# Performance work log

Measured on AMD Instinct MI355X. Metric: run time of the kernel, lower is better.

## Reference

```python
import math
import jax, jax.numpy as jnp
import numpy as np

N, D = 16384, 1024


def setup_inputs() -> dict:
    key = jax.random.key(0)
    k1, k2 = jax.random.split(key)
    return {
        "image_embeddings_aligned": jax.random.normal(k1, (N, D), dtype=jnp.float32),
        "text_embeddings_aligned": jax.random.normal(k2, (N, D), dtype=jnp.float32),
        "logit_scale": jnp.asarray(math.log(20.0), dtype=jnp.float32),  # stored as log(init)
        "logit_bias": jnp.asarray(-10.0, dtype=jnp.float32),
    }


def _l2_normalize(x, eps=1e-12):
    # matches F.normalize(p=2, dim=-1)
    n = jnp.linalg.norm(x, axis=-1, keepdims=True)
    return x / jnp.maximum(n, eps)


def reference(image_embeddings_aligned, text_embeddings_aligned, logit_scale, logit_bias):
    img = _l2_normalize(image_embeddings_aligned)
    txt = _l2_normalize(text_embeddings_aligned)
    # [N, N] pairwise logits
    logits = jnp.exp(logit_scale) * jnp.einsum("nd,md->nm", img, txt) + logit_bias
    n = logits.shape[0]
    labels = 2.0 * jnp.eye(n, dtype=logits.dtype) - 1.0  # +1 on diagonal, -1 off
    loss_matrix = jax.nn.log_sigmoid(labels * logits)
    siglip_loss = -jnp.mean(loss_matrix)  # total_loss (structure_lambda == 0)
    return siglip_loss
```

## Files before the change

### kernel.cpp

```cpp
#include <hip/hip_runtime.h>

#define NROWS 16384
#define DIM   1024
#define QSCALE 32.0f
#define E8M0S  0x7A7A7A7Au

typedef int    v4i    __attribute__((ext_vector_type(4)));
typedef int    v8i    __attribute__((ext_vector_type(8)));
typedef float  f32x16 __attribute__((ext_vector_type(16)));

__device__ __forceinline__ void glds16(const void* g, void* l) {
    __builtin_amdgcn_global_load_lds(
        (const __attribute__((address_space(1))) void*)g,
        (__attribute__((address_space(3))) void*)l,
        16, 0, 0);
}

__device__ __forceinline__ float fexp2(float x) {
#if __has_builtin(__builtin_amdgcn_exp2f)
    return __builtin_amdgcn_exp2f(x);
#else
    return exp2f(x);
#endif
}
__device__ __forceinline__ float flog2(float x) {
#if __has_builtin(__builtin_amdgcn_logf)
    return __builtin_amdgcn_logf(x);
#else
    return log2f(x);
#endif
}

__device__ __forceinline__ unsigned fp4_nib(float y) {
    unsigned s = (__float_as_uint(y) >> 31) << 3;
    float a = fminf(fabsf(y), 6.0f);
    unsigned c = (unsigned)(a >= 0.25f) + (unsigned)(a >= 0.75f) +
                 (unsigned)(a >= 1.25f) + (unsigned)(a >= 1.75f) +
                 (unsigned)(a >= 2.5f)  + (unsigned)(a >= 3.5f)  +
                 (unsigned)(a >= 5.0f);
    return c | s;
}

__global__ __launch_bounds__(256) void norm_fused(
    const float* __restrict__ img,
    const float* __restrict__ txt,
    unsigned char* __restrict__ imgQ,
    unsigned char* __restrict__ txtQ,
    const float* __restrict__ lscale,
    const float* __restrict__ lbias,
    float* __restrict__ diagPart) {
    const int t    = threadIdx.x;
    const int lane = t & 63;
    const int r31  = lane & 31;
    const int half = lane >> 5;
    const int gw   = blockIdx.x * 4 + (t >> 6);
    const int row  = gw * 2 + half;
    const float sc   = __expf(lscale[0]);
    const float bias = lbias[0];

    const float4* pi = (const float4*)(img + (size_t)row * DIM) + r31 * 8;
    const float4* pt = (const float4*)(txt + (size_t)row * DIM) + r31 * 8;
    float4 vi[8], vt[8];
    float ssi = 0.0f, sst = 0.0f, dot = 0.0f;
    #pragma unroll
    for (int j = 0; j < 8; ++j) {
        vi[j] = pi[j];
        vt[j] = pt[j];
        ssi += vi[j].x*vi[j].x + vi[j].y*vi[j].y + vi[j].z*vi[j].z + vi[j].w*vi[j].w;
        sst += vt[j].x*vt[j].x + vt[j].y*vt[j].y + vt[j].z*vt[j].z + vt[j].w*vt[j].w;
        dot += vi[j].x*vt[j].x + vi[j].y*vt[j].y + vi[j].z*vt[j].z + vi[j].w*vt[j].w;
    }
    #pragma unroll
    for (int off = 1; off < 32; off <<= 1) {
        ssi += __shfl_xor(ssi, off, 64);
        sst += __shfl_xor(sst, off, 64);
        dot += __shfl_xor(dot, off, 64);
    }
    const float ii = 1.0f / fmaxf(sqrtf(ssi), 1e-12f);
    const float it = 1.0f / fmaxf(sqrtf(sst), 1e-12f);
    if (r31 == 0) diagPart[row] = -fmaf(sc, dot * ii * it, bias);

    const float qi = ii * QSCALE, qt = it * QSCALE;
    unsigned wp[4] = {0, 0, 0, 0}, wq[4] = {0, 0, 0, 0};
    #pragma unroll
    for (int j = 0; j < 8; ++j) {
        unsigned p = fp4_nib(vi[j].x * qi)       | (fp4_nib(vi[j].y * qi) << 4) |
                     (fp4_nib(vi[j].z * qi) << 8) | (fp4_nib(vi[j].w * qi) << 12);
        unsigned q = fp4_nib(vt[j].x * qt)       | (fp4_nib(vt[j].y * qt) << 4) |
                     (fp4_nib(vt[j].z * qt) << 8) | (fp4_nib(vt[j].w * qt) << 12);
        wp[j >> 1] |= p << ((j & 1) * 16);
        wq[j >> 1] |= q << ((j & 1) * 16);
    }
    const size_t qoff = ((size_t)(row >> 5) * 32 + r31) * 512 + (row & 31) * 16;
    *(v4i*)(imgQ + qoff) = *(v4i*)wp;
    *(v4i*)(txtQ + qoff) = *(v4i*)wq;
}

__global__ __launch_bounds__(256, 4) void siglip_gemm(
    const unsigned char* __restrict__ A,
    const unsigned char* __restrict__ B,
    const float* __restrict__ lscale,
    const float* __restrict__ lbias,
    float* __restrict__ gemmPart)
{
    __shared__ unsigned char sA[2][16 * 1024];
    __shared__ float wred[4];

    const int t    = threadIdx.x;
    const int lane = t & 63;
    const int wave = t >> 6;
    const int wr   = wave >> 1;
    const int wc   = wave & 1;

    const int b    = blockIdx.x;
    const int xcd  = b & 7;
    const int lb   = b >> 3;
    const int bcol = xcd * 16 + (lb & 15);
    const int brow = lb >> 4;

    const unsigned char* Aw = A + ((size_t)(brow * 4 + wave) * 32) * 512
                                + (size_t)lane * 16;
    const unsigned char* Bw = B + ((size_t)(bcol * 4 + wc * 2) * 32) * 512
                                + (size_t)lane * 16;

    f32x16 acc[2][2] = {};

    #pragma unroll
    for (int s = 0; s < 4; ++s)
        glds16(Aw + (size_t)(s * 2) * 512, sA[0] + (wave * 8 + s * 2) * 512);
    __syncthreads();

    #pragma unroll
    for (int k = 0; k < 4; ++k) {
        const int cur = k & 1;

        if (k < 3) {
            #pragma unroll
            for (int s = 0; s < 4; ++s)
                glds16(Aw + (size_t)((k + 1) * 8 + s * 2) * 512,
                       sA[cur ^ 1] + (wave * 8 + s * 2) * 512);
        }

        v4i bc0 = *(const v4i*)(Bw + (size_t)(k * 8) * 512);
        v4i bc1 = *(const v4i*)(Bw + 16384 + (size_t)(k * 8) * 512);

        #pragma unroll
        for (int ks = 0; ks < 4; ++ks) {
            v4i bn0, bn1;
            if (ks < 3) {
                bn0 = *(const v4i*)(Bw + (size_t)(k * 8 + (ks + 1) * 2) * 512);
                bn1 = *(const v4i*)(Bw + 16384 + (size_t)(k * 8 + (ks + 1) * 2) * 512);
            }
            v4i a0 = *(const v4i*)(sA[cur] + ((2 * wr + 0) * 8 + ks * 2) * 512 + lane * 16);
            v4i a1 = *(const v4i*)(sA[cur] + ((2 * wr + 1) * 8 + ks * 2) * 512 + lane * 16);

            v8i A0 = __builtin_shufflevector(a0, a0, 0, 1, 2, 3, -1, -1, -1, -1);
            v8i A1 = __builtin_shufflevector(a1, a1, 0, 1, 2, 3, -1, -1, -1, -1);
            v8i B0 = __builtin_shufflevector(bc0, bc0, 0, 1, 2, 3, -1, -1, -1, -1);
            v8i B1 = __builtin_shufflevector(bc1, bc1, 0, 1, 2, 3, -1, -1, -1, -1);

            __builtin_amdgcn_s_setprio(1);
            acc[0][0] = __builtin_amdgcn_mfma_scale_f32_32x32x64_f8f6f4(
                A0, B0, acc[0][0], 4, 4, 0, (int)E8M0S, 0, (int)E8M0S);
            acc[0][1] = __builtin_amdgcn_mfma_scale_f32_32x32x64_f8f6f4(
                A0, B1, acc[0][1], 4, 4, 0, (int)E8M0S, 0, (int)E8M0S);
            acc[1][0] = __builtin_amdgcn_mfma_scale_f32_32x32x64_f8f6f4(
                A1, B0, acc[1][0], 4, 4, 0, (int)E8M0S, 0, (int)E8M0S);
            acc[1][1] = __builtin_amdgcn_mfma_scale_f32_32x32x64_f8f6f4(
                A1, B1, acc[1][1], 4, 4, 0, (int)E8M0S, 0, (int)E8M0S);
            __builtin_amdgcn_s_setprio(0);

            if (ks < 3) { bc0 = bn0; bc1 = bn1; }
        }

        __syncthreads();
    }

    const float l2e   = 1.44269504088896341f;
    const float scale = __expf(lscale[0]);
    const float aCo   = scale * l2e;
    const float bCo   = lbias[0] * l2e;
    float local = 0.0f;
    #pragma unroll
    for (int mi = 0; mi < 2; ++mi)
        #pragma unroll
        for (int ni = 0; ni < 2; ++ni)
            #pragma unroll
            for (int r = 0; r < 16; r += 4) {
                float e0 = fexp2(fmaf(aCo, acc[mi][ni][r + 0], bCo));
                float e1 = fexp2(fmaf(aCo, acc[mi][ni][r + 1], bCo));
                float e2 = fexp2(fmaf(aCo, acc[mi][ni][r + 2], bCo));
                float e3 = fexp2(fmaf(aCo, acc[mi][ni][r + 3], bCo));
                float p  = ((1.0f + e0) * (1.0f + e1)) *
                           ((1.0f + e2) * (1.0f + e3));
                local += flog2(p);
            }

    #pragma unroll
    for (int off = 32; off > 0; off >>= 1) local += __shfl_down(local, off, 64);
    if (lane == 0) wred[wave] = local;
    __syncthreads();
    if (t == 0)
        gemmPart[blockIdx.x] =
            (wred[0] + wred[1] + wred[2] + wred[3]) * 0.69314718055994531f;
}

__global__ __launch_bounds__(1024) void finalize_kernel(
    const float* __restrict__ parts, float* __restrict__ out) {
    __shared__ float wr[16];
    const int t    = threadIdx.x;
    const int lane = t & 63;
    const int wave = t >> 6;
    const float4* p4 = (const float4*)parts;
    float s = 0.0f;
    for (int i = t; i < 8192; i += 1024) {
        float4 v = p4[i];
        s += v.x + v.y + v.z + v.w;
    }
    #pragma unroll
    for (int off = 32; off > 0; off >>= 1) s += __shfl_down(s, off, 64);
    if (lane == 0) wr[wave] = s;
    __syncthreads();
    if (t == 0) {
        float tot = 0.0f;
        #pragma unroll
        for (int i = 0; i < 16; ++i) tot += wr[i];
        out[0] = tot / 268435456.0f;
    }
}

extern "C" void kernel_launch(void* const* d_in, const int* in_sizes, int n_in,
                              void* d_out, int out_size, void* d_ws, size_t ws_size,
                              hipStream_t stream) {
    const float* img    = (const float*)d_in[0];
    const float* txt    = (const float*)d_in[1];
    const float* lscale = (const float*)d_in[2];
    const float* lbias  = (const float*)d_in[3];
    float* out = (float*)d_out;

    char* ws = (char*)d_ws;
    unsigned char* imgQ = (unsigned char*)ws;
    unsigned char* txtQ = (unsigned char*)(ws + (size_t)NROWS * 512);
    float* parts   = (float*)(ws + (size_t)2 * NROWS * 512);
    float* diagPart = parts;
    float* gemmPart = parts + NROWS;

    norm_fused<<<2048, 256, 0, stream>>>(img, txt, imgQ, txtQ, lscale, lbias, diagPart);
    siglip_gemm<<<dim3((NROWS / 128) * (NROWS / 128)), 256, 0, stream>>>(
        imgQ, txtQ, lscale, lbias, gemmPart);
    finalize_kernel<<<1, 1024, 0, stream>>>(parts, out);
}
```

Before: 313.1 us.

## Load A fragments directly from global into registers, dropping LDS staging

Removes the LDS double buffer and global_load_lds staging for the A operand. Each wave now loads both A and B fragments straight from global memory into registers, with a one-step register prefetch across a 16-step K loop, so the __syncthreads barriers go away. This cuts LDS traffic and synchronisation, but each A tile is now fetched by two waves instead of being shared through LDS, which doubles global/L2 reads for A.

Result: no change. 310.1 us (-1.0%).

```diff
diff --git a/kernel.cpp b/kernel.cpp
--- a/kernel.cpp
+++ b/kernel.cpp
@@ -8,13 +8,6 @@
 typedef int    v4i    __attribute__((ext_vector_type(4)));
 typedef int    v8i    __attribute__((ext_vector_type(8)));
 typedef float  f32x16 __attribute__((ext_vector_type(16)));
-
-__device__ __forceinline__ void glds16(const void* g, void* l) {
-    __builtin_amdgcn_global_load_lds(
-        (const __attribute__((address_space(1))) void*)g,
-        (__attribute__((address_space(3))) void*)l,
-        16, 0, 0);
-}
 
 __device__ __forceinline__ float fexp2(float x) {
 #if __has_builtin(__builtin_amdgcn_exp2f)
@@ -103,14 +96,13 @@
     const float* __restrict__ lbias,
     float* __restrict__ gemmPart)
 {
-    __shared__ unsigned char sA[2][16 * 1024];
     __shared__ float wred[4];
 
     const int t    = threadIdx.x;
     const int lane = t & 63;
     const int wave = t >> 6;
-    const int wr   = wave >> 1;
-    const int wc   = wave & 1;
+    const int wy   = wave >> 1;
+    const int wx   = wave & 1;
 
     const int b    = blockIdx.x;
     const int xcd  = b & 7;
@@ -118,62 +110,46 @@
     const int bcol = xcd * 16 + (lb & 15);
     const int brow = lb >> 4;
 
-    const unsigned char* Aw = A + ((size_t)(brow * 4 + wave) * 32) * 512
+    const unsigned char* Ab = A + (size_t)(brow * 4 + wy * 2) * 16384
                                 + (size_t)lane * 16;
-    const unsigned char* Bw = B + ((size_t)(bcol * 4 + wc * 2) * 32) * 512
+    const unsigned char* Bb = B + (size_t)(bcol * 4 + wx * 2) * 16384
                                 + (size_t)lane * 16;
 
     f32x16 acc[2][2] = {};
 
-    #pragma unroll
-    for (int s = 0; s < 4; ++s)
-        glds16(Aw + (size_t)(s * 2) * 512, sA[0] + (wave * 8 + s * 2) * 512);
-    __syncthreads();
-
-    #pragma unroll
-    for (int k = 0; k < 4; ++k) {
-        const int cur = k & 1;
-
-        if (k < 3) {
-            #pragma unroll
-            for (int s = 0; s < 4; ++s)
-                glds16(Aw + (size_t)((k + 1) * 8 + s * 2) * 512,
-                       sA[cur ^ 1] + (wave * 8 + s * 2) * 512);
+    v4i a0 = *(const v4i*)(Ab);
+    v4i a1 = *(const v4i*)(Ab + 16384);
+    v4i b0 = *(const v4i*)(Bb);
+    v4i b1 = *(const v4i*)(Bb + 16384);
+
+    #pragma unroll
+    for (int s = 0; s < 16; ++s) {
+        v4i na0, na1, nb0, nb1;
+        if (s < 15) {
+            const int o = (s + 1) * 1024;
+            na0 = *(const v4i*)(Ab + o);
+            na1 = *(const v4i*)(Ab + 16384 + o);
+            nb0 = *(const v4i*)(Bb + o);
+            nb1 = *(const v4i*)(Bb + 16384 + o);
         }
 
-        v4i bc0 = *(const v4i*)(Bw + (size_t)(k * 8) * 512);
-        v4i bc1 = *(const v4i*)(Bw + 16384 + (size_t)(k * 8) * 512);
-
-        #pragma unroll
-        for (int ks = 0; ks < 4; ++ks) {
-            v4i bn0, bn1;
-            if (ks < 3) {
-                bn0 = *(const v4i*)(Bw + (size_t)(k * 8 + (ks + 1) * 2) * 512);
-                bn1 = *(const v4i*)(Bw + 16384 + (size_t)(k * 8 + (ks + 1) * 2) * 512);
-            }
-            v4i a0 = *(const v4i*)(sA[cur] + ((2 * wr + 0) * 8 + ks * 2) * 512 + lane * 16);
-            v4i a1 = *(const v4i*)(sA[cur] + ((2 * wr + 1) * 8 + ks * 2) * 512 + lane * 16);
-
-            v8i A0 = __builtin_shufflevector(a0, a0, 0, 1, 2, 3, -1, -1, -1, -1);
-            v8i A1 = __builtin_shufflevector(a1, a1, 0, 1, 2, 3, -1, -1, -1, -1);
-            v8i B0 = __builtin_shufflevector(bc0, bc0, 0, 1, 2, 3, -1, -1, -1, -1);
-            v8i B1 = __builtin_shufflevector(bc1, bc1, 0, 1, 2, 3, -1, -1, -1, -1);
-
-            __builtin_amdgcn_s_setprio(1);
-            acc[0][0] = __builtin_amdgcn_mfma_scale_f32_32x32x64_f8f6f4(
-                A0, B0, acc[0][0], 4, 4, 0, (int)E8M0S, 0, (int)E8M0S);
-            acc[0][1] = __builtin_amdgcn_mfma_scale_f32_32x32x64_f8f6f4(
-                A0, B1, acc[0][1], 4, 4, 0, (int)E8M0S, 0, (int)E8M0S);
-            acc[1][0] = __builtin_amdgcn_mfma_scale_f32_32x32x64_f8f6f4(
-                A1, B0, acc[1][0], 4, 4, 0, (int)E8M0S, 0, (int)E8M0S);
-            acc[1][1] = __builtin_amdgcn_mfma_scale_f32_32x32x64_f8f6f4(
-                A1, B1, acc[1][1], 4, 4, 0, (int)E8M0S, 0, (int)E8M0S);
-            __builtin_amdgcn_s_setprio(0);
-
-            if (ks < 3) { bc0 = bn0; bc1 = bn1; }
-        }
-
-        __syncthreads();
+        v8i A0 = __builtin_shufflevector(a0, a0, 0, 1, 2, 3, -1, -1, -1, -1);
+        v8i A1 = __builtin_shufflevector(a1, a1, 0, 1, 2, 3, -1, -1, -1, -1);
+        v8i B0 = __builtin_shufflevector(b0, b0, 0, 1, 2, 3, -1, -1, -1, -1);
+        v8i B1 = __builtin_shufflevector(b1, b1, 0, 1, 2, 3, -1, -1, -1, -1);
+
+        __builtin_amdgcn_s_setprio(1);
+        acc[0][0] = __builtin_amdgcn_mfma_scale_f32_32x32x64_f8f6f4(
+            A0, B0, acc[0][0], 4, 4, 0, (int)E8M0S, 0, (int)E8M0S);
+        acc[0][1] = __builtin_amdgcn_mfma_scale_f32_32x32x64_f8f6f4(
+            A0, B1, acc[0][1], 4, 4, 0, (int)E8M0S, 0, (int)E8M0S);
+        acc[1][0] = __builtin_amdgcn_mfma_scale_f32_32x32x64_f8f6f4(
+            A1, B0, acc[1][0], 4, 4, 0, (int)E8M0S, 0, (int)E8M0S);
+        acc[1][1] = __builtin_amdgcn_mfma_scale_f32_32x32x64_f8f6f4(
+            A1, B1, acc[1][1], 4, 4, 0, (int)E8M0S, 0, (int)E8M0S);
+        __builtin_amdgcn_s_setprio(0);
+
+        if (s < 15) { a0 = na0; a1 = na1; b0 = nb0; b1 = nb1; }
     }
 
     const float l2e   = 1.44269504088896341f;
```
